# Optimization experiments

Measured on AMD Instinct MI355X. Metric: run time of the kernel, lower is better.

The kernel has to match this reference:

```python
import jax, jax.numpy as jnp
import numpy as np

EMB = 768
HEADS = 12
DEPTH = EMB // HEADS
B, L = 8, 1024


def setup_inputs() -> dict:
    key = jax.random.key(0)
    ks = jax.random.split(key, 11)
    s = 1.0 / np.sqrt(EMB)
    inp = {
        "v": jax.random.normal(ks[0], (B, L, EMB), jnp.float32),
        "k": jax.random.normal(ks[1], (B, L, EMB), jnp.float32),
        "q": jax.random.normal(ks[2], (B, L, EMB), jnp.float32),
        # torch Linear weights: [out_features, in_features]
        "wq_w": jax.random.normal(ks[3], (EMB, EMB), jnp.float32) * s,
        "wq_b": jax.random.normal(ks[4], (EMB,), jnp.float32) * s,
        "wk_w": jax.random.normal(ks[5], (EMB, EMB), jnp.float32) * s,
        "wk_b": jax.random.normal(ks[6], (EMB,), jnp.float32) * s,
        "wv_w": jax.random.normal(ks[7], (EMB, EMB), jnp.float32) * s,
        "wv_b": jax.random.normal(ks[8], (EMB,), jnp.float32) * s,
        "dense_w": jax.random.normal(ks[9], (EMB, EMB), jnp.float32) * s,
        "dense_b": jax.random.normal(ks[10], (EMB,), jnp.float32) * s,
    }
    return inp


def _split_heads(x):
    b, l, _ = x.shape
    return x.reshape(b, l, HEADS, DEPTH).transpose(0, 2, 1, 3)  # [b,h,l,d]


def reference(v, k, q, wq_w, wq_b, wk_w, wk_b, wv_w, wv_b, dense_w, dense_b):
    qh = _split_heads(q @ wq_w.T + wq_b)
    kh = _split_heads(k @ wk_w.T + wk_b)
    vh = _split_heads(v @ wv_w.T + wv_b)
    # NOTE: module scales by sqrt(embedding_dim), not sqrt(depth)
    scale = 1.0 / jnp.sqrt(jnp.asarray(EMB, qh.dtype))
    score = jnp.einsum("bhqd,bhkd->bhqk", qh, kh) * scale
    attn_w = jax.nn.softmax(score, axis=-1)  # [b,h,lq,lk]
    logits = jnp.einsum("bhqk,bhkd->bhqd", attn_w, vh)
    concat = logits.transpose(0, 2, 1, 3).reshape(q.shape[0], -1, EMB)
    attention = concat @ dense_w.T + dense_b  # dropout p=0 -> identity
    return attention, attn_w
```

## Files before the change

kernel.cpp:

```cpp
#include <hip/hip_runtime.h>

#define EMB 768
#define NH 12
#define HD 64
#define BBATCH 8
#define LL 1024
#define BL (BBATCH * LL)

typedef __attribute__((ext_vector_type(8))) short bf16x8;
typedef __attribute__((ext_vector_type(4))) float f32x4;

__device__ __forceinline__ unsigned int f2bfu(float f) {
  unsigned int u = __builtin_bit_cast(unsigned int, f);
  return (u + 0x7FFFu + ((u >> 16) & 1u)) >> 16;
}

__device__ __forceinline__ f32x4 mfma16(bf16x8 a, bf16x8 b, f32x4 c) {
  return __builtin_amdgcn_mfma_f32_16x16x32_bf16(a, b, c, 0, 0, 0);
}

__global__ __launch_bounds__(256) void convert_w_kernel(
    const float* __restrict__ wq, const float* __restrict__ wk,
    const float* __restrict__ wv, const float* __restrict__ wd,
    unsigned short* __restrict__ out) {
  const int n = EMB * EMB;
  int e = (blockIdx.x * 256 + threadIdx.x) * 4;
  int which = e / n;
  int off = e - which * n;
  const float* src = (which == 0) ? wq : (which == 1) ? wk : (which == 2) ? wv : wd;
  float4 v4 = *reinterpret_cast<const float4*>(src + off);
  uint2 o;
  o.x = f2bfu(v4.x) | (f2bfu(v4.y) << 16);
  o.y = f2bfu(v4.z) | (f2bfu(v4.w) << 16);
  *reinterpret_cast<uint2*>(out + e) = o;
}

template <int MODE>
__global__ __launch_bounds__(256) void gemm_xwt_kernel(
    const void* __restrict__ Xv, const unsigned short* __restrict__ W,
    const float* __restrict__ bias, void* __restrict__ outp, float out_scale) {
  constexpr bool IN_F32 = (MODE != 2);
  extern __shared__ char smem[];
  unsigned short* Ab = reinterpret_cast<unsigned short*>(smem);
  unsigned short* Bb = Ab + 128 * 32;

  const int t = threadIdx.x;
  const int lane = t & 63, wid = t >> 6;
  const int wr = wid >> 1, wc = wid & 1;
  const int lrow = lane & 15, lgrp = lane >> 4;
  const int bm0 = blockIdx.x * 128, bn0 = blockIdx.y * 128;

  f32x4 acc[4][4];
#pragma unroll
  for (int i = 0; i < 4; ++i)
#pragma unroll
    for (int j = 0; j < 4; ++j) acc[i][j] = (f32x4){0.f, 0.f, 0.f, 0.f};

  float4 aF[2][2];
  uint4 aB[2];
  uint4 bB[2];

  const int ar = t >> 2, as = t & 3;
  const int rb = t >> 1, sb = (t & 1) * 2;

  auto load_regs = [&](int kt) {
    const int k0 = kt * 32;
    if constexpr (IN_F32) {
      const float* X = reinterpret_cast<const float*>(Xv);
      const float* g0 = X + (size_t)(bm0 + ar) * EMB + k0 + as * 8;
      aF[0][0] = reinterpret_cast<const float4*>(g0)[0];
      aF[0][1] = reinterpret_cast<const float4*>(g0)[1];
      const float* g1 = g0 + (size_t)64 * EMB;
      aF[1][0] = reinterpret_cast<const float4*>(g1)[0];
      aF[1][1] = reinterpret_cast<const float4*>(g1)[1];
    } else {
      const unsigned short* X = reinterpret_cast<const unsigned short*>(Xv);
      const uint4* g = reinterpret_cast<const uint4*>(X + (size_t)(bm0 + rb) * EMB + k0 + sb * 8);
      aB[0] = g[0];
      aB[1] = g[1];
    }
    const uint4* gw = reinterpret_cast<const uint4*>(W + (size_t)(bn0 + rb) * EMB + k0 + sb * 8);
    bB[0] = gw[0];
    bB[1] = gw[1];
  };

  auto write_lds = [&]() {
    if constexpr (IN_F32) {
#pragma unroll
      for (int it = 0; it < 2; ++it) {
        int r = ar + it * 64;
        uint4 pk;
        pk.x = f2bfu(aF[it][0].x) | (f2bfu(aF[it][0].y) << 16);
        pk.y = f2bfu(aF[it][0].z) | (f2bfu(aF[it][0].w) << 16);
        pk.z = f2bfu(aF[it][1].x) | (f2bfu(aF[it][1].y) << 16);
        pk.w = f2bfu(aF[it][1].z) | (f2bfu(aF[it][1].w) << 16);
        *reinterpret_cast<uint4*>(Ab + r * 32 + ((as ^ (r & 3)) * 8)) = pk;
      }
    } else {
      *reinterpret_cast<uint4*>(Ab + rb * 32 + ((sb ^ (rb & 3)) * 8)) = aB[0];
      *reinterpret_cast<uint4*>(Ab + rb * 32 + (((sb + 1) ^ (rb & 3)) * 8)) = aB[1];
    }
    *reinterpret_cast<uint4*>(Bb + rb * 32 + ((sb ^ (rb & 3)) * 8)) = bB[0];
    *reinterpret_cast<uint4*>(Bb + rb * 32 + (((sb + 1) ^ (rb & 3)) * 8)) = bB[1];
  };

  auto compute = [&]() {
    bf16x8 a[4], b[4];
    const int sw = (lgrp ^ (lrow & 3)) * 8;
#pragma unroll
    for (int i = 0; i < 4; ++i) {
      int r = wr * 64 + i * 16 + lrow;
      a[i] = *reinterpret_cast<const bf16x8*>(Ab + r * 32 + sw);
      int c = wc * 64 + i * 16 + lrow;
      b[i] = *reinterpret_cast<const bf16x8*>(Bb + c * 32 + sw);
    }
#pragma unroll
    for (int i = 0; i < 4; ++i)
#pragma unroll
      for (int j = 0; j < 4; ++j) acc[i][j] = mfma16(a[i], b[j], acc[i][j]);
  };

  load_regs(0);
  write_lds();
  __syncthreads();
#pragma unroll 1
  for (int kt = 0; kt < 24; ++kt) {
    if (kt < 23) load_regs(kt + 1);
    compute();
    __syncthreads();
    if (kt < 23) {
      write_lds();
      __syncthreads();
    }
  }

  if constexpr (MODE == 0) {
    unsigned short* out = reinterpret_cast<unsigned short*>(outp);
#pragma unroll
    for (int jj = 0; jj < 4; ++jj) {
      int C = bn0 + wc * 64 + jj * 16 + lrow;
      float bv = bias[C];
      int hh = C >> 6, dd = C & 63;
#pragma unroll
      for (int i = 0; i < 4; ++i)
#pragma unroll
        for (int j2 = 0; j2 < 4; ++j2) {
          int R = bm0 + wr * 64 + i * 16 + lgrp * 4 + j2;
          int bidx = R >> 10, l = R & 1023;
          out[(((size_t)(bidx * NH + hh) * 1024 + l) << 6) + dd] =
              (unsigned short)f2bfu((acc[i][jj][j2] + bv) * out_scale);
        }
    }
  }

  if constexpr (MODE == 1) {
    __syncthreads();
    unsigned short* T = reinterpret_cast<unsigned short*>(smem);
#pragma unroll
    for (int jj = 0; jj < 4; ++jj) {
      int cl = wc * 64 + jj * 16 + lrow;
      float bv = bias[bn0 + cl];
#pragma unroll
      for (int i = 0; i < 4; ++i)
#pragma unroll
        for (int j2 = 0; j2 < 4; ++j2) {
          int rl = wr * 64 + i * 16 + lgrp * 4 + j2;
          T[cl * 136 + rl] = (unsigned short)f2bfu(acc[i][jj][j2] + bv);
        }
    }
    __syncthreads();
    unsigned short* out = reinterpret_cast<unsigned short*>(outp);
    int cl = t >> 1, rh = (t & 1) * 64;
    int C = bn0 + cl, hh = C >> 6, dd = C & 63;
    int Rg = bm0 + rh, bidx = Rg >> 10, l0 = Rg & 1023;
    size_t obase = ((size_t)(bidx * NH + hh) * 64 + dd) * 1024 + l0;
#pragma unroll
    for (int q8 = 0; q8 < 8; ++q8) {
      uint4 val = *reinterpret_cast<const uint4*>(T + cl * 136 + rh + q8 * 8);
      *reinterpret_cast<uint4*>(out + obase + q8 * 8) = val;
    }
  }

  if constexpr (MODE == 2) {
    float* out = reinterpret_cast<float*>(outp);
#pragma unroll
    for (int jj = 0; jj < 4; ++jj) {
      int C = bn0 + wc * 64 + jj * 16 + lrow;
      float bv = bias[C];
#pragma unroll
      for (int i = 0; i < 4; ++i)
#pragma unroll
        for (int j2 = 0; j2 < 4; ++j2) {
          int R = bm0 + wr * 64 + i * 16 + lgrp * 4 + j2;
          out[(size_t)R * EMB + C] = acc[i][jj][j2] + bv;
        }
    }
  }
}

__global__ __launch_bounds__(256) void attn_kernel(
    const unsigned short* __restrict__ qh, const unsigned short* __restrict__ kh,
    const unsigned short* __restrict__ vhT, float* __restrict__ attn_w,
    unsigned short* __restrict__ concat) {
  __shared__ unsigned short Pl[16 * 1024];
  __shared__ float red[2][4][16];

  const int t = threadIdx.x;
  const int lane = t & 63, w = t >> 6;
  const int lrow = lane & 15, lgrp = lane >> 4;
  const int qt = blockIdx.x, pair = blockIdx.y;
  const int b = pair / NH, h = pair - b * NH;
  const int q0 = qt * 16;
  const unsigned short* qbase = qh + (size_t)pair * (LL * HD);
  const unsigned short* kbase = kh + (size_t)pair * (LL * HD);
  const unsigned short* vbase = vhT + (size_t)pair * (HD * LL);

  bf16x8 aq[2];
#pragma unroll
  for (int c = 0; c < 2; ++c)
    aq[c] = *reinterpret_cast<const bf16x8*>(qbase + (size_t)(q0 + lrow) * HD + c * 32 + lgrp * 8);

  f32x4 acc[16];
#pragma unroll
  for (int f = 0; f < 16; ++f) acc[f] = (f32x4){0.f, 0.f, 0.f, 0.f};

  const int k0 = w * 256;
  __builtin_amdgcn_s_setprio(1);
#pragma unroll
  for (int f = 0; f < 16; ++f) {
    const unsigned short* kr = kbase + (size_t)(k0 + f * 16 + lrow) * HD + lgrp * 8;
    bf16x8 b0 = *reinterpret_cast<const bf16x8*>(kr);
    bf16x8 b1 = *reinterpret_cast<const bf16x8*>(kr + 32);
    acc[f] = mfma16(b0, aq[0], acc[f]);
    acc[f] = mfma16(b1, aq[1], acc[f]);
  }
  __builtin_amdgcn_s_setprio(0);

  const unsigned short* vrow = vbase + (size_t)(w * 16 + lrow) * LL;
  bf16x8 vpre[8];
#pragma unroll
  for (int kk = 0; kk < 8; ++kk)
    vpre[kk] = *reinterpret_cast<const bf16x8*>(vrow + kk * 32 + lgrp * 8);

  float m = acc[0][0];
#pragma unroll
  for (int f = 0; f < 16; ++f)
#pragma unroll
    for (int j = 0; j < 4; ++j) m = fmaxf(m, acc[f][j]);
  m = fmaxf(m, __shfl_xor(m, 16));
  m = fmaxf(m, __shfl_xor(m, 32));
  if (lane < 16) red[0][w][lane] = m;
  __syncthreads();
  float M = fmaxf(fmaxf(red[0][0][lrow], red[0][1][lrow]),
                  fmaxf(red[0][2][lrow], red[0][3][lrow]));
  float s = 0.f;
#pragma unroll
  for (int f = 0; f < 16; ++f)
#pragma unroll
    for (int j = 0; j < 4; ++j) {
      float p = __expf(acc[f][j] - M);
      acc[f][j] = p;
      s += p;
    }
  s += __shfl_xor(s, 16);
  s += __shfl_xor(s, 32);
  if (lane < 16) red[1][w][lane] = s;
  __syncthreads();
  float inv = 1.0f / (red[1][0][lrow] + red[1][1][lrow] + red[1][2][lrow] + red[1][3][lrow]);

  float* awp = attn_w + (size_t)pair * (LL * LL) + (size_t)(q0 + lrow) * LL + k0 + lgrp * 4;
  char* Plb = reinterpret_cast<char*>(Pl);
#pragma unroll
  for (int f = 0; f < 16; ++f) {
    float p0 = acc[f][0] * inv, p1 = acc[f][1] * inv;
    float p2 = acc[f][2] * inv, p3 = acc[f][3] * inv;
    f32x4 o = {p0, p1, p2, p3};
    *reinterpret_cast<f32x4*>(awp + f * 16) = o;
    uint2 pb;
    pb.x = f2bfu(p0) | (f2bfu(p1) << 16);
    pb.y = f2bfu(p2) | (f2bfu(p3) << 16);
    int byte = (lrow * 2048 + (k0 + f * 16 + lgrp * 4) * 2) ^ ((lrow & 7) << 4);
    *reinterpret_cast<uint2*>(Plb + byte) = pb;
  }
  __syncthreads();

  f32x4 o = (f32x4){0.f, 0.f, 0.f, 0.f};
  __builtin_amdgcn_s_setprio(1);
#pragma unroll
  for (int kk = 0; kk < 32; ++kk) {
    int byte = (lrow * 2048 + (kk * 32 + lgrp * 8) * 2) ^ ((lrow & 7) << 4);
    bf16x8 pa = *reinterpret_cast<const bf16x8*>(Plb + byte);
    bf16x8 vb = (kk < 8) ? vpre[kk]
                         : *reinterpret_cast<const bf16x8*>(vrow + kk * 32 + lgrp * 8);
    o = mfma16(pa, vb, o);
  }
  __builtin_amdgcn_s_setprio(0);
#pragma unroll
  for (int j = 0; j < 4; ++j) {
    int row = q0 + lgrp * 4 + j;
    int cc = h * 64 + w * 16 + lrow;
    concat[((size_t)b * LL + row) * EMB + cc] = (unsigned short)f2bfu(o[j]);
  }
}

extern "C" void kernel_launch(void* const* d_in, const int* in_sizes, int n_in,
                              void* d_out, int out_size, void* d_ws, size_t ws_size,
                              hipStream_t stream) {
  const float* v = (const float*)d_in[0];
  const float* k = (const float*)d_in[1];
  const float* q = (const float*)d_in[2];
  const float* wq_w = (const float*)d_in[3];
  const float* wq_b = (const float*)d_in[4];
  const float* wk_w = (const float*)d_in[5];
  const float* wk_b = (const float*)d_in[6];
  const float* wv_w = (const float*)d_in[7];
  const float* wv_b = (const float*)d_in[8];
  const float* dw = (const float*)d_in[9];
  const float* db = (const float*)d_in[10];

  float* out_attn = (float*)d_out;
  float* out_w = out_attn + (size_t)BL * EMB;

  if (ws_size < 55050240u) return;
  unsigned short* ws = (unsigned short*)d_ws;
  unsigned short* wqb16 = ws;
  unsigned short* wkb16 = wqb16 + EMB * EMB;
  unsigned short* wvb16 = wkb16 + EMB * EMB;
  unsigned short* wdb16 = wvb16 + EMB * EMB;
  unsigned short* qhb = wdb16 + EMB * EMB;
  unsigned short* khb = qhb + (size_t)BL * EMB;
  unsigned short* vtb = khb + (size_t)BL * EMB;
  unsigned short* cat = vtb + (size_t)BL * EMB;

  convert_w_kernel<<<dim3(2304), dim3(256), 0, stream>>>(wq_w, wk_w, wv_w, dw, ws);

  const float scale = 0.036084391824351615f;
  dim3 gg(64, 6);
  gemm_xwt_kernel<0><<<gg, 256, 16384, stream>>>(q, wqb16, wq_b, qhb, scale);
  gemm_xwt_kernel<0><<<gg, 256, 16384, stream>>>(k, wkb16, wk_b, khb, 1.0f);
  gemm_xwt_kernel<1><<<gg, 256, 128 * 136 * 2, stream>>>(v, wvb16, wv_b, vtb, 1.0f);

  attn_kernel<<<dim3(64, 96), dim3(256), 0, stream>>>(qhb, khb, vtb, out_w, cat);

  gemm_xwt_kernel<2><<<gg, 256, 16384, stream>>>(cat, wdb16, db, out_attn, 1.0f);
}
```

Measured before the change: 426.9 us.

## Stage attention-weight tile through LDS for fully coalesced row stores

Normalized probabilities are first written to a shared-memory fp32 buffer, in two halves of 8 rows each, and then stored to attn_w as contiguous 1 KB rows per wavefront. The previous layout wrote scattered 16-byte chunks per lane. The goal is fully coalesced global writes for the large attention-weight output, which dominates memory traffic. The change also removes the s_setprio hints and adds 32 KB of LDS plus extra barriers, which can reduce occupancy.

```diff
diff --git a/kernel.cpp b/kernel.cpp
--- a/kernel.cpp
+++ b/kernel.cpp
@@ -203,6 +203,7 @@
     const unsigned short* __restrict__ vhT, float* __restrict__ attn_w,
     unsigned short* __restrict__ concat) {
   __shared__ unsigned short Pl[16 * 1024];
+  __shared__ float Sf[8 * 1024];
   __shared__ float red[2][4][16];
 
   const int t = threadIdx.x;
@@ -225,7 +226,6 @@
   for (int f = 0; f < 16; ++f) acc[f] = (f32x4){0.f, 0.f, 0.f, 0.f};
 
   const int k0 = w * 256;
-  __builtin_amdgcn_s_setprio(1);
 #pragma unroll
   for (int f = 0; f < 16; ++f) {
     const unsigned short* kr = kbase + (size_t)(k0 + f * 16 + lrow) * HD + lgrp * 8;
@@ -234,13 +234,12 @@
     acc[f] = mfma16(b0, aq[0], acc[f]);
     acc[f] = mfma16(b1, aq[1], acc[f]);
   }
-  __builtin_amdgcn_s_setprio(0);
-
-  const unsigned short* vrow = vbase + (size_t)(w * 16 + lrow) * LL;
+
+  const unsigned short* vrow = vbase + (size_t)(w * 16 + lrow) * LL + lgrp * 8;
   bf16x8 vpre[8];
 #pragma unroll
   for (int kk = 0; kk < 8; ++kk)
-    vpre[kk] = *reinterpret_cast<const bf16x8*>(vrow + kk * 32 + lgrp * 8);
+    vpre[kk] = *reinterpret_cast<const bf16x8*>(vrow + kk * 32);
 
   float m = acc[0][0];
 #pragma unroll
@@ -268,33 +267,72 @@
   __syncthreads();
   float inv = 1.0f / (red[1][0][lrow] + red[1][1][lrow] + red[1][2][lrow] + red[1][3][lrow]);
 
-  float* awp = attn_w + (size_t)pair * (LL * LL) + (size_t)(q0 + lrow) * LL + k0 + lgrp * 4;
   char* Plb = reinterpret_cast<char*>(Pl);
+  char* Sfb = reinterpret_cast<char*>(Sf);
+  const int br = lrow & 7;
 #pragma unroll
   for (int f = 0; f < 16; ++f) {
     float p0 = acc[f][0] * inv, p1 = acc[f][1] * inv;
     float p2 = acc[f][2] * inv, p3 = acc[f][3] * inv;
-    f32x4 o = {p0, p1, p2, p3};
-    *reinterpret_cast<f32x4*>(awp + f * 16) = o;
+    acc[f][0] = p0; acc[f][1] = p1; acc[f][2] = p2; acc[f][3] = p3;
     uint2 pb;
     pb.x = f2bfu(p0) | (f2bfu(p1) << 16);
     pb.y = f2bfu(p2) | (f2bfu(p3) << 16);
     int byte = (lrow * 2048 + (k0 + f * 16 + lgrp * 4) * 2) ^ ((lrow & 7) << 4);
     *reinterpret_cast<uint2*>(Plb + byte) = pb;
-  }
-  __syncthreads();
+    if (lrow < 8) {
+      int sb = (br * 4096 + (k0 + f * 16 + lgrp * 4) * 4) ^ (br << 4);
+      *reinterpret_cast<f32x4*>(Sfb + sb) = (f32x4){p0, p1, p2, p3};
+    }
+  }
+  __syncthreads();
+
+  float* awbase = attn_w + (size_t)pair * (LL * LL) + (size_t)q0 * LL;
+#pragma unroll
+  for (int rr = 0; rr < 2; ++rr) {
+    int r = w * 2 + rr;
+    float* dst = awbase + (size_t)r * LL;
+#pragma unroll
+    for (int c = 0; c < 4; ++c) {
+      int sb = (r * 4096 + c * 1024 + lane * 16) ^ ((r & 7) << 4);
+      f32x4 val = *reinterpret_cast<const f32x4*>(Sfb + sb);
+      *reinterpret_cast<f32x4*>(dst + c * 256 + lane * 4) = val;
+    }
+  }
 
   f32x4 o = (f32x4){0.f, 0.f, 0.f, 0.f};
-  __builtin_amdgcn_s_setprio(1);
 #pragma unroll
   for (int kk = 0; kk < 32; ++kk) {
     int byte = (lrow * 2048 + (kk * 32 + lgrp * 8) * 2) ^ ((lrow & 7) << 4);
     bf16x8 pa = *reinterpret_cast<const bf16x8*>(Plb + byte);
     bf16x8 vb = (kk < 8) ? vpre[kk]
-                         : *reinterpret_cast<const bf16x8*>(vrow + kk * 32 + lgrp * 8);
+                         : *reinterpret_cast<const bf16x8*>(vrow + kk * 32);
     o = mfma16(pa, vb, o);
   }
-  __builtin_amdgcn_s_setprio(0);
+  __syncthreads();
+
+  if (lrow >= 8) {
+#pragma unroll
+    for (int f = 0; f < 16; ++f) {
+      int sb = (br * 4096 + (k0 + f * 16 + lgrp * 4) * 4) ^ (br << 4);
+      *reinterpret_cast<f32x4*>(Sfb + sb) =
+          (f32x4){acc[f][0], acc[f][1], acc[f][2], acc[f][3]};
+    }
+  }
+  __syncthreads();
+
+#pragma unroll
+  for (int rr = 0; rr < 2; ++rr) {
+    int r = w * 2 + rr;
+    float* dst = awbase + (size_t)(8 + r) * LL;
+#pragma unroll
+    for (int c = 0; c < 4; ++c) {
+      int sb = (r * 4096 + c * 1024 + lane * 16) ^ ((r & 7) << 4);
+      f32x4 val = *reinterpret_cast<const f32x4*>(Sfb + sb);
+      *reinterpret_cast<f32x4*>(dst + c * 256 + lane * 4) = val;
+    }
+  }
+
 #pragma unroll
   for (int j = 0; j < 4; ++j) {
     int row = q0 + lgrp * 4 + j;
```

New measurement: 486.8 us. 1.14x slower.
